# Kernel optimization log

Hardware: AMD Instinct MI355X
Metric: run time of the kernel (lower is better)

## Reference

```python
import jax, jax.numpy as jnp
import numpy as np


def setup_inputs() -> dict:
    key = jax.random.key(0)
    k1, k2, *kw = jax.random.split(key, 12)
    N, E = 10000, 320000
    D_IN, D_HID, D_EMB, D_PRED = 2, 128, 256, 128

    def lin(k, fan_in, fan_out):
        bound = 1.0 / np.sqrt(fan_in)
        kw_, kb_ = jax.random.split(k)
        W = jax.random.uniform(kw_, (fan_in, fan_out), jnp.float32, -bound, bound)
        b = jax.random.uniform(kb_, (fan_out,), jnp.float32, -bound, bound)
        return W, b

    W1, b1 = lin(kw[0], D_IN, D_HID)
    W2, b2 = lin(kw[1], D_HID, D_EMB)
    Wp1, bp1 = lin(kw[2], D_EMB, D_PRED)
    Wp2, bp2 = lin(kw[3], D_PRED, 1)

    src = jax.random.randint(k1, (E,), 0, N, dtype=jnp.int32)
    dst = jax.random.randint(k2, (E,), 0, N, dtype=jnp.int32)
    return {
        "W1": W1, "b1": b1, "W2": W2, "b2": b2,
        "Wp1": Wp1, "bp1": bp1, "Wp2": Wp2, "bp2": bp2,
        "src": src, "dst": dst, "num_nodes": N,
    }


def reference(W1, b1, W2, b2, Wp1, bp1, Wp2, bp2, src, dst, num_nodes):
    N = num_nodes
    E = src.shape[0]
    ones = jnp.ones((E,), jnp.float32)
    # node features = [in_degree, out_degree]  -> [N, 2]
    in_deg = jax.ops.segment_sum(ones, dst, num_segments=N)
    out_deg = jax.ops.segment_sum(ones, src, num_segments=N)
    x = jnp.stack([in_deg, out_deg], axis=1)

    def gcn_agg(h):
        # sum of messages from source nodes into destination nodes (SpMM-like)
        return jax.ops.segment_sum(h[src], dst, num_segments=N)

    h = jax.nn.relu(gcn_agg(x) @ W1 + b1)        # [N, 128]
    h = gcn_agg(h) @ W2 + b2                     # [N, 256]
    h = jax.nn.relu(h)
    graph_embedding = jnp.sum(h, axis=0)         # [256] (dgl.sum_nodes, single graph)
    m = jax.nn.relu(graph_embedding @ Wp1 + bp1)
    metric = m @ Wp2 + bp2                       # [1]
    return (graph_embedding, metric)
```

## Files before the change

kernel.cpp:

```cpp
#include <hip/hip_runtime.h>

#define N_NODES 10000
#define CAPLOG 7
#define CAP 128
#define NPART 16

__global__ __launch_bounds__(256) void bucket_kernel(const int* __restrict__ src,
                                                     const int* __restrict__ dst,
                                                     unsigned int* __restrict__ pack,
                                                     int* __restrict__ slots, int E) {
  int e = blockIdx.x * 256 + threadIdx.x;
  if (e < E) {
    int s = src[e], d = dst[e];
    unsigned old = atomicAdd(&pack[d], 1u);
    atomicAdd(&pack[s], 0x10000u);
    unsigned idx = old & 0xFFFFu;
    if (idx < CAP) slots[(d << CAPLOG) + idx] = s;
  }
}

__global__ __launch_bounds__(256) void agg1_kernel(const unsigned int* __restrict__ pack,
                                                   const int* __restrict__ slots,
                                                   float2* __restrict__ a) {
  const int tid = threadIdx.x;
  const int hw = tid >> 5, hl = tid & 31;
  const int node = blockIdx.x * 8 + hw;
  const int deg = min((int)(pack[node] & 0xFFFFu), CAP);
  const int base = node << CAPLOG;
  float a0 = 0.f, a1 = 0.f;
  for (int e = hl; e < deg; e += 32) {
    unsigned v = pack[slots[base + e]];
    a0 += (float)(v & 0xFFFFu);
    a1 += (float)(v >> 16);
  }
#pragma unroll
  for (int off = 16; off > 0; off >>= 1) {
    a0 += __shfl_xor(a0, off);
    a1 += __shfl_xor(a1, off);
  }
  if (hl == 0) a[node] = make_float2(a0, a1);
}

__global__ __launch_bounds__(256) void agg2gemm2_kernel(const unsigned int* __restrict__ pack,
                                                        const int* __restrict__ slots,
                                                        const float2* __restrict__ a,
                                                        const float* __restrict__ W1,
                                                        const float* __restrict__ b1,
                                                        const float* __restrict__ W2,
                                                        const float* __restrict__ b2,
                                                        float* __restrict__ ge_p) {
  __shared__ float s_tile[8][128];
  const int tid = threadIdx.x, bid = blockIdx.x;
  const int hw = tid >> 5, hl = tid & 31;

  float w10[4], w11[4], bb[4];
#pragma unroll
  for (int c = 0; c < 4; ++c) {
    w10[c] = W1[4 * hl + c];
    w11[c] = W1[128 + 4 * hl + c];
    bb[c] = b1[4 * hl + c];
  }
  const int node = bid * 8 + hw;
  const int deg = min((int)(pack[node] & 0xFFFFu), CAP);
  float acc0 = 0.f, acc1 = 0.f, acc2 = 0.f, acc3 = 0.f;
  int rem = deg, eb = node << CAPLOG;
  while (rem > 0) {
    int cnt = min(rem, 32);
    float va0 = 0.f, va1 = 0.f;
    if (hl < cnt) {
      float2 av = a[slots[eb + hl]];
      va0 = av.x;
      va1 = av.y;
    }
    for (int j = 0; j < cnt; ++j) {
      float x0 = __shfl(va0, j, 32);
      float x1 = __shfl(va1, j, 32);
      acc0 += fmaxf(fmaf(x0, w10[0], fmaf(x1, w11[0], bb[0])), 0.f);
      acc1 += fmaxf(fmaf(x0, w10[1], fmaf(x1, w11[1], bb[1])), 0.f);
      acc2 += fmaxf(fmaf(x0, w10[2], fmaf(x1, w11[2], bb[2])), 0.f);
      acc3 += fmaxf(fmaf(x0, w10[3], fmaf(x1, w11[3], bb[3])), 0.f);
    }
    rem -= cnt;
    eb += cnt;
  }
  s_tile[hw][4 * hl + 0] = acc0;
  s_tile[hw][4 * hl + 1] = acc1;
  s_tile[hw][4 * hl + 2] = acc2;
  s_tile[hw][4 * hl + 3] = acc3;
  __syncthreads();

  float d[8];
#pragma unroll
  for (int n = 0; n < 8; ++n) d[n] = 0.f;
#pragma unroll
  for (int kc = 0; kc < 4; ++kc) {
    float wv[32];
#pragma unroll
    for (int c = 0; c < 32; ++c) wv[c] = W2[(kc * 32 + c) * 256 + tid];
#pragma unroll
    for (int n = 0; n < 8; ++n) {
      const float4* row4 = (const float4*)&s_tile[n][kc * 32];
      float t0 = 0.f, t1 = 0.f, t2 = 0.f, t3 = 0.f;
#pragma unroll
      for (int q = 0; q < 8; ++q) {
        float4 rv = row4[q];
        t0 = fmaf(rv.x, wv[4 * q + 0], t0);
        t1 = fmaf(rv.y, wv[4 * q + 1], t1);
        t2 = fmaf(rv.z, wv[4 * q + 2], t2);
        t3 = fmaf(rv.w, wv[4 * q + 3], t3);
      }
      d[n] += (t0 + t1) + (t2 + t3);
    }
  }

  const float bj = b2[tid];
  float accge = 0.f;
#pragma unroll
  for (int n = 0; n < 8; ++n) accge += fmaxf(d[n] + bj, 0.f);
  atomicAdd(&ge_p[((bid & (NPART - 1)) << 8) + tid], accge);
}

__global__ __launch_bounds__(256) void head_kernel(const float* __restrict__ ge_p,
                                                   const float* __restrict__ Wp1,
                                                   const float* __restrict__ bp1,
                                                   const float* __restrict__ Wp2,
                                                   const float* __restrict__ bp2,
                                                   float* __restrict__ out) {
  __shared__ float s_ge[256];
  __shared__ float s_m[256];
  int tid = threadIdx.x;
  float g = 0.f;
#pragma unroll
  for (int p = 0; p < NPART; ++p) g += ge_p[p * 256 + tid];
  s_ge[tid] = g;
  out[tid] = g;
  __syncthreads();
  int j = tid & 127, halfk = tid >> 7;
  float d = halfk ? 0.f : bp1[j];
  int k0 = halfk << 7;
#pragma unroll 8
  for (int k = k0; k < k0 + 128; ++k) d = fmaf(s_ge[k], Wp1[k * 128 + j], d);
  s_m[tid] = d;
  __syncthreads();
  if (tid < 128) s_m[tid] = fmaxf(s_m[tid] + s_m[tid + 128], 0.f) * Wp2[tid];
  __syncthreads();
  if (tid < 64) {
    float v = s_m[tid] + s_m[tid + 64];
#pragma unroll
    for (int off = 32; off > 0; off >>= 1) v += __shfl_xor(v, off);
    if (tid == 0) out[256] = v + bp2[0];
  }
}

extern "C" void kernel_launch(void* const* d_in, const int* in_sizes, int n_in,
                              void* d_out, int out_size, void* d_ws, size_t ws_size,
                              hipStream_t stream) {
  const float* W1 = (const float*)d_in[0];
  const float* b1 = (const float*)d_in[1];
  const float* W2 = (const float*)d_in[2];
  const float* b2 = (const float*)d_in[3];
  const float* Wp1 = (const float*)d_in[4];
  const float* bp1 = (const float*)d_in[5];
  const float* Wp2 = (const float*)d_in[6];
  const float* bp2 = (const float*)d_in[7];
  const int* src = (const int*)d_in[8];
  const int* dst = (const int*)d_in[9];
  const int E = in_sizes[8];
  const int N = N_NODES;

  char* p = (char*)d_ws;
  unsigned int* pack = (unsigned int*)p; p += (size_t)N * 4;
  float* ge_p = (float*)p;               p += (size_t)NPART * 256 * 4;
  int* slots = (int*)p;                  p += (size_t)N * CAP * 4;
  float2* a = (float2*)p;
  float* out = (float*)d_out;

  hipMemsetAsync(d_ws, 0, ((size_t)N + NPART * 256) * 4, stream);

  bucket_kernel<<<(E + 255) / 256, 256, 0, stream>>>(src, dst, pack, slots, E);
  agg1_kernel<<<N / 8, 256, 0, stream>>>(pack, slots, a);
  agg2gemm2_kernel<<<N / 8, 256, 0, stream>>>(pack, slots, a, W1, b1, W2, b2, ge_p);
  head_kernel<<<1, 256, 0, stream>>>(ge_p, Wp1, bp1, Wp2, bp2, out);
}
```

Baseline: 149.7 us.

## Replace global-atomic bucketing with shared-memory histogram, scan, and scatter

The single bucket kernel, which did global atomics per edge, is replaced by three kernels. A per-block LDS histogram computes in- and out-degrees, a per-node scan over the 128 block histograms gives per-block offsets, and a scatter kernel places source ids using LDS atomics. Slots shrink to 16-bit indices, halving slot-array traffic. This trades contended global atomics for two extra launches and about 10 MB of partial-count and offset arrays in global memory.

```diff
diff --git a/kernel.cpp b/kernel.cpp
--- a/kernel.cpp
+++ b/kernel.cpp
@@ -4,23 +4,63 @@
 #define CAPLOG 7
 #define CAP 128
 #define NPART 16
-
-__global__ __launch_bounds__(256) void bucket_kernel(const int* __restrict__ src,
-                                                     const int* __restrict__ dst,
-                                                     unsigned int* __restrict__ pack,
-                                                     int* __restrict__ slots, int E) {
-  int e = blockIdx.x * 256 + threadIdx.x;
-  if (e < E) {
-    int s = src[e], d = dst[e];
-    unsigned old = atomicAdd(&pack[d], 1u);
-    atomicAdd(&pack[s], 0x10000u);
-    unsigned idx = old & 0xFFFFu;
-    if (idx < CAP) slots[(d << CAPLOG) + idx] = s;
+#define NBH 128
+#define TBH 512
+
+__global__ __launch_bounds__(TBH) void hist_kernel(const int* __restrict__ src,
+                                                   const int* __restrict__ dst,
+                                                   unsigned int* __restrict__ cnt, int E) {
+  __shared__ unsigned int hist[N_NODES];
+  const int tid = threadIdx.x, bid = blockIdx.x;
+  for (int i = tid; i < N_NODES; i += TBH) hist[i] = 0;
+  __syncthreads();
+  const int chunk = (E + NBH - 1) / NBH;
+  const int e0 = bid * chunk, e1 = min(E, e0 + chunk);
+  for (int e = e0 + tid; e < e1; e += TBH) {
+    atomicAdd(&hist[dst[e]], 1u);
+    atomicAdd(&hist[src[e]], 0x10000u);
+  }
+  __syncthreads();
+  unsigned int* outb = cnt + (size_t)bid * N_NODES;
+  for (int i = tid; i < N_NODES; i += TBH) outb[i] = hist[i];
+}
+
+__global__ __launch_bounds__(256) void scan_kernel(const unsigned int* __restrict__ cnt,
+                                                   unsigned int* __restrict__ off,
+                                                   unsigned int* __restrict__ pack) {
+  const int n = blockIdx.x * 256 + threadIdx.x;
+  if (n >= N_NODES) return;
+  unsigned run_in = 0, run_out = 0;
+  for (int b = 0; b < NBH; ++b) {
+    unsigned v = cnt[(size_t)b * N_NODES + n];
+    off[(size_t)b * N_NODES + n] = run_in;
+    run_in += v & 0xFFFFu;
+    run_out += v >> 16;
+  }
+  pack[n] = run_in | (run_out << 16);
+}
+
+__global__ __launch_bounds__(TBH) void scatter_kernel(const int* __restrict__ src,
+                                                      const int* __restrict__ dst,
+                                                      const unsigned int* __restrict__ off,
+                                                      unsigned short* __restrict__ slots,
+                                                      int E) {
+  __shared__ unsigned int cur[N_NODES];
+  const int tid = threadIdx.x, bid = blockIdx.x;
+  const unsigned int* ob = off + (size_t)bid * N_NODES;
+  for (int i = tid; i < N_NODES; i += TBH) cur[i] = ob[i];
+  __syncthreads();
+  const int chunk = (E + NBH - 1) / NBH;
+  const int e0 = bid * chunk, e1 = min(E, e0 + chunk);
+  for (int e = e0 + tid; e < e1; e += TBH) {
+    int d = dst[e];
+    unsigned idx = atomicAdd(&cur[d], 1u);
+    if (idx < CAP) slots[(d << CAPLOG) + idx] = (unsigned short)src[e];
   }
 }
 
 __global__ __launch_bounds__(256) void agg1_kernel(const unsigned int* __restrict__ pack,
-                                                   const int* __restrict__ slots,
+                                                   const unsigned short* __restrict__ slots,
                                                    float2* __restrict__ a) {
   const int tid = threadIdx.x;
   const int hw = tid >> 5, hl = tid & 31;
@@ -42,7 +82,7 @@
 }
 
 __global__ __launch_bounds__(256) void agg2gemm2_kernel(const unsigned int* __restrict__ pack,
-                                                        const int* __restrict__ slots,
+                                                        const unsigned short* __restrict__ slots,
                                                         const float2* __restrict__ a,
                                                         const float* __restrict__ W1,
                                                         const float* __restrict__ b1,
@@ -169,15 +209,19 @@
   const int N = N_NODES;
 
   char* p = (char*)d_ws;
+  float* ge_p = (float*)p;               p += (size_t)NPART * 256 * 4;
   unsigned int* pack = (unsigned int*)p; p += (size_t)N * 4;
-  float* ge_p = (float*)p;               p += (size_t)NPART * 256 * 4;
-  int* slots = (int*)p;                  p += (size_t)N * CAP * 4;
-  float2* a = (float2*)p;
+  unsigned short* slots = (unsigned short*)p; p += (size_t)N * CAP * 2;
+  float2* a = (float2*)p;                p += (size_t)N * 8;
+  unsigned int* cnt = (unsigned int*)p;  p += (size_t)NBH * N * 4;
+  unsigned int* off = (unsigned int*)p;
   float* out = (float*)d_out;
 
-  hipMemsetAsync(d_ws, 0, ((size_t)N + NPART * 256) * 4, stream);
-
-  bucket_kernel<<<(E + 255) / 256, 256, 0, stream>>>(src, dst, pack, slots, E);
+  hipMemsetAsync(d_ws, 0, (size_t)NPART * 256 * 4, stream);
+
+  hist_kernel<<<NBH, TBH, 0, stream>>>(src, dst, cnt, E);
+  scan_kernel<<<(N + 255) / 256, 256, 0, stream>>>(cnt, off, pack);
+  scatter_kernel<<<NBH, TBH, 0, stream>>>(src, dst, off, slots, E);
   agg1_kernel<<<N / 8, 256, 0, stream>>>(pack, slots, a);
   agg2gemm2_kernel<<<N / 8, 256, 0, stream>>>(pack, slots, a, W1, b1, W2, b2, ge_p);
   head_kernel<<<1, 256, 0, stream>>>(ge_p, Wp1, bp1, Wp2, bp2, out);
```

Result: faster. 132.4 us (-11.5%).
